# Kernel tuning notes

Hardware: AMD Instinct MI355X
Metric: run time of the kernel (lower is better)

Reference implementation:

```python
import jax, jax.numpy as jnp
import numpy as np

HEADS = 16
D_MODEL = 1024
HEAD_DIM = D_MODEL // HEADS


def setup_inputs() -> dict:
    key = jax.random.key(0)
    ks = jax.random.split(key, 11)
    B, S = 4, 2048
    scale_in = 1.0 / np.sqrt(HEAD_DIM)
    scale_out = 1.0 / np.sqrt(D_MODEL)
    return {
        "values": jax.random.normal(ks[0], (B, S, D_MODEL), dtype=jnp.float32),
        "keys": jax.random.normal(ks[1], (B, S, D_MODEL), dtype=jnp.float32),
        "query": jax.random.normal(ks[2], (B, S, D_MODEL), dtype=jnp.float32),
        "wq": jax.random.normal(ks[3], (HEAD_DIM, HEAD_DIM), dtype=jnp.float32) * scale_in,
        "bq": jax.random.normal(ks[4], (HEAD_DIM,), dtype=jnp.float32) * 0.01,
        "wk": jax.random.normal(ks[5], (HEAD_DIM, HEAD_DIM), dtype=jnp.float32) * scale_in,
        "bk": jax.random.normal(ks[6], (HEAD_DIM,), dtype=jnp.float32) * 0.01,
        "wv": jax.random.normal(ks[7], (HEAD_DIM, HEAD_DIM), dtype=jnp.float32) * scale_in,
        "bv": jax.random.normal(ks[8], (HEAD_DIM,), dtype=jnp.float32) * 0.01,
        "wo": jax.random.normal(ks[9], (D_MODEL, D_MODEL), dtype=jnp.float32) * scale_out,
        "bo": jax.random.normal(ks[10], (D_MODEL,), dtype=jnp.float32) * 0.01,
    }


def reference(values, keys, query, wq, bq, wk, bk, wv, bv, wo, bo):
    B, Sq = query.shape[0], query.shape[1]
    Sk, Sv = keys.shape[1], values.shape[1]
    # reshape to (n, s, h, d); per-head linear shares one [d,d] weight across heads
    v = values.reshape(B, Sv, HEADS, HEAD_DIM) @ wv.T + bv
    k = keys.reshape(B, Sk, HEADS, HEAD_DIM) @ wk.T + bk
    q = query.reshape(B, Sq, HEADS, HEAD_DIM) @ wq.T + bq
    # scores scaled by sqrt(d_model) (as in original, NOT sqrt(head_dim))
    energy = jnp.einsum("nqhd,nkhd->nhqk", q, k)
    attn = jax.nn.softmax(energy / jnp.sqrt(jnp.float32(D_MODEL)), axis=-1)
    out = jnp.einsum("nhqk,nkhd->nqhd", attn, v).reshape(B, Sq, D_MODEL)
    return out @ wo.T + bo
```

## Files before the change

### kernel.cpp

```cpp
#include <hip/hip_runtime.h>

typedef unsigned short u16;
typedef short  bfrag  __attribute__((ext_vector_type(8), may_alias));
typedef unsigned long long ull_a __attribute__((may_alias));
typedef int    int_a  __attribute__((may_alias));
typedef int    i4_a   __attribute__((ext_vector_type(4), may_alias));
typedef float  f4_a   __attribute__((ext_vector_type(4), may_alias));
typedef __attribute__((ext_vector_type(4)))  float facc4;
typedef __attribute__((ext_vector_type(16))) float facc16;

#define SEQ   2048
#define NHEAD 16
#define HD    64
#define DM    1024
#define BH    64
#define NTOK  8192
#define QSC   0.04508422f

#if defined(__has_builtin)
#if __has_builtin(__builtin_amdgcn_cvt_pk_bf16_f32)
#define HAS_CVT_PK 1
#endif
#endif
#ifndef HAS_CVT_PK
#define HAS_CVT_PK 0
#endif

__device__ __forceinline__ u16 f2bf(float f){
  union { float f; unsigned u; } x; x.f = f;
  unsigned r = x.u + 0x7FFFu + ((x.u >> 16) & 1u);
  return (u16)(r >> 16);
}
__device__ __forceinline__ unsigned pk2(float a, float b){
#if HAS_CVT_PK
  auto r = __builtin_amdgcn_cvt_pk_bf16_f32(a, b);
  union { decltype(r) v; unsigned u; } x; x.v = r; return x.u;
#else
  return (unsigned)f2bf(a) | ((unsigned)f2bf(b) << 16);
#endif
}
__device__ __forceinline__ unsigned long long pk4(float a, float b, float c, float d){
  return (unsigned long long)pk2(a,b) | ((unsigned long long)pk2(c,d) << 32);
}
__device__ __forceinline__ bfrag ld8f(const float* p){
  f4_a a = *(const f4_a*)p;
  f4_a b = *(const f4_a*)(p + 4);
  union { bfrag v; unsigned u[4]; } r;
  r.u[0] = pk2(a[0],a[1]); r.u[1] = pk2(a[2],a[3]);
  r.u[2] = pk2(b[0],b[1]); r.u[3] = pk2(b[2],b[3]);
  return r.v;
}
__device__ __forceinline__ void stage16(const u16* g, u16* l){
  __builtin_amdgcn_global_load_lds((const __attribute__((address_space(1))) void*)g,
                                   (__attribute__((address_space(3))) void*)l, 16, 0, 0);
}

__global__ __launch_bounds__(256) void k_wconv(
  const float* __restrict__ wo, const float* __restrict__ wq,
  const float* __restrict__ wk, const float* __restrict__ wv,
  u16* __restrict__ dst)
{
  long i = ((long)blockIdx.x * 256 + threadIdx.x) * 8;
  const float* src; long off;
  if      (i < 1048576)        { src = wo; off = i; }
  else if (i < 1048576+4096)   { src = wq; off = i - 1048576; }
  else if (i < 1048576+8192)   { src = wk; off = i - (1048576+4096); }
  else                         { src = wv; off = i - (1048576+8192); }
  f4_a a = *(const f4_a*)(src + off);
  f4_a b = *(const f4_a*)(src + off + 4);
  ull_a* p = (ull_a*)(dst + i);
  p[0] = pk4(a[0],a[1],a[2],a[3]);
  p[1] = pk4(b[0],b[1],b[2],b[3]);
}

__global__ __launch_bounds__(256) void k_proj(
  const float* __restrict__ vin, const float* __restrict__ kin, const float* __restrict__ qin,
  const u16* __restrict__ wqb, const u16* __restrict__ wkb, const u16* __restrict__ wvb,
  const float* __restrict__ bq, const float* __restrict__ bk, const float* __restrict__ bv,
  u16* __restrict__ qo, u16* __restrict__ ko, u16* __restrict__ vo)
{
  __shared__ __align__(16) u16 Lq[16*264], Lk[16*264], Lv[16*264];
  int tid  = threadIdx.x;
  int wid  = tid >> 6, lane = tid & 63;
  int quad = lane >> 4, col = lane & 15;
  int token = blockIdx.x * 4 + wid;
  int b  = (blockIdx.x * 4) >> 11;
  int s0 = (blockIdx.x * 4) & 2047;
  long xbase = (long)token * DM;

  bfrag aq[2], ak[2], av[2];
  #pragma unroll
  for (int ks = 0; ks < 2; ks++){
    long off = xbase + (long)col * HD + ks*32 + quad*8;
    aq[ks] = ld8f(qin + off);
    ak[ks] = ld8f(kin + off);
    av[ks] = ld8f(vin + off);
  }
  #pragma unroll
  for (int ns = 0; ns < 4; ns++){
    facc4 accq = {0.f,0.f,0.f,0.f}, acck = {0.f,0.f,0.f,0.f}, accv = {0.f,0.f,0.f,0.f};
    #pragma unroll
    for (int ks = 0; ks < 2; ks++){
      int woff = (ns*16 + col) * HD + ks*32 + quad*8;
      bfrag bwq = *(const bfrag*)(wqb + woff);
      bfrag bwk = *(const bfrag*)(wkb + woff);
      bfrag bwv = *(const bfrag*)(wvb + woff);
      accq = __builtin_amdgcn_mfma_f32_16x16x32_bf16(aq[ks], bwq, accq, 0,0,0);
      acck = __builtin_amdgcn_mfma_f32_16x16x32_bf16(ak[ks], bwk, acck, 0,0,0);
      accv = __builtin_amdgcn_mfma_f32_16x16x32_bf16(av[ks], bwv, accv, 0,0,0);
    }
    int d = ns*16 + col;
    float fbq = bq[d], fbk = bk[d], fbv = bv[d];
    #pragma unroll
    for (int r = 0; r < 4; r++){
      int h = quad*4 + r;
      int li = h*264 + wid*64 + d;
      Lq[li] = f2bf((accq[r] + fbq) * QSC);
      Lk[li] = f2bf(acck[r] + fbk);
      Lv[li] = f2bf(accv[r] + fbv);
    }
  }
  __syncthreads();
  int h = tid >> 4, c = tid & 15;
  int src = h*264 + c*16;
  long gb = ((long)(b*NHEAD + h) * SEQ + s0) * HD + c*16;
  *(i4_a*)(qo + gb)     = *(const i4_a*)&Lq[src];
  *(i4_a*)(qo + gb + 8) = *(const i4_a*)&Lq[src + 8];
  *(i4_a*)(ko + gb)     = *(const i4_a*)&Lk[src];
  *(i4_a*)(ko + gb + 8) = *(const i4_a*)&Lk[src + 8];
  *(i4_a*)(vo + gb)     = *(const i4_a*)&Lv[src];
  *(i4_a*)(vo + gb + 8) = *(const i4_a*)&Lv[src + 8];
}

__global__ __launch_bounds__(256) void k_vtrans(
  const u16* __restrict__ vin, u16* __restrict__ vt)
{
  __shared__ __align__(16) u16 T[64*264];
  int tid = threadIdx.x;
  int wid = tid >> 6, lane = tid & 63;
  int s0  = blockIdx.x * 256;
  int bh  = blockIdx.y;
  const u16* ip = vin + ((long)bh * SEQ + s0 + tid) * HD;
  #pragma unroll
  for (int j = 0; j < 8; j++){
    bfrag v8 = *(const bfrag*)(ip + j*8);
    #pragma unroll
    for (int i = 0; i < 8; i++)
      T[(j*8 + i)*264 + tid] = (u16)((short*)&v8)[i];
  }
  __syncthreads();
  long obase = (long)bh * HD * SEQ + s0;
  #pragma unroll
  for (int it = 0; it < 16; it++){
    int d = it*4 + wid;
    ull_a v = *(const ull_a*)&T[d*264 + lane*4];
    *(ull_a*)(vt + obase + (long)d * SEQ + lane*4) = v;
  }
}

__global__ __launch_bounds__(256, 3) void k_attn(
  const u16* __restrict__ qws, const u16* __restrict__ kws, const u16* __restrict__ vt,
  u16* __restrict__ aout)
{
  __shared__ __align__(16) u16 KV[2][2][64*64];
  __shared__ __align__(16) u16 Pt[4][32*72];
  int tid = threadIdx.x;
  int wid = tid >> 6, lane = tid & 63;
  int ln = lane & 31, hh = lane >> 5;
  int bh = blockIdx.y;
  int q0 = blockIdx.x * 128 + wid * 32;
  long base = (long)bh * SEQ * HD;

  int srow   = lane >> 3;
  int schunk = (lane & 7) ^ srow;

  bfrag qf[4];
  #pragma unroll
  for (int ks = 0; ks < 4; ks++)
    qf[ks] = *(const bfrag*)(qws + base + (long)(q0 + ln)*HD + ks*16 + hh*8);

  facc16 OO0, OO1;
  #pragma unroll
  for (int r = 0; r < 16; r++){ OO0[r] = 0.f; OO1[r] = 0.f; }
  float l_ = 0.f;

  #pragma unroll
  for (int g2 = 0; g2 < 2; g2++){
    int g = wid + g2*4;
    stage16(kws + base + (long)(g*8 + srow)*HD + schunk*8,       &KV[0][0][g*512]);
    stage16(vt  + base + (long)(g*8 + srow)*SEQ + schunk*8,      &KV[0][1][g*512]);
  }

  for (int kt = 0; kt < 32; kt++){
    int buf = kt & 1;
    __syncthreads();
    if (kt + 1 < 32){
      int k0n = (kt + 1) * 64;
      #pragma unroll
      for (int g2 = 0; g2 < 2; g2++){
        int g = wid + g2*4;
        stage16(kws + base + (long)(k0n + g*8 + srow)*HD + schunk*8, &KV[buf^1][0][g*512]);
        stage16(vt  + base + (long)(g*8 + srow)*SEQ + k0n + schunk*8, &KV[buf^1][1][g*512]);
      }
    }

    facc16 E0, E1;
    #pragma unroll
    for (int r = 0; r < 16; r++){ E0[r] = 0.f; E1[r] = 0.f; }
    #pragma unroll
    for (int ks = 0; ks < 4; ks++){
      int sw = ((2*ks + hh) ^ (ln & 7)) * 8;
      bfrag kf0 = *(const bfrag*)&KV[buf][0][ ln      *64 + sw];
      bfrag kf1 = *(const bfrag*)&KV[buf][0][(32 + ln)*64 + sw];
      E0 = __builtin_amdgcn_mfma_f32_32x32x16_bf16(kf0, qf[ks], E0, 0,0,0);
      E1 = __builtin_amdgcn_mfma_f32_32x32x16_bf16(kf1, qf[ks], E1, 0,0,0);
    }

    float rs = 0.f;
    #pragma unroll
    for (int r = 0; r < 16; r++){
      float p0 = __builtin_amdgcn_exp2f(E0[r]);
      float p1 = __builtin_amdgcn_exp2f(E1[r]);
      E0[r] = p0; E1[r] = p1; rs += p0 + p1;
    }
    rs += __shfl_xor(rs, 32, 64);
    l_ += rs;

    u16* pw = &Pt[wid][ln*72];
    #pragma unroll
    for (int g = 0; g < 4; g++){
      *(ull_a*)(pw +      8*g + 4*hh) = pk4(E0[4*g], E0[4*g+1], E0[4*g+2], E0[4*g+3]);
      *(ull_a*)(pw + 32 + 8*g + 4*hh) = pk4(E1[4*g], E1[4*g+1], E1[4*g+2], E1[4*g+3]);
    }

    bfrag pf[4];
    #pragma unroll
    for (int ks = 0; ks < 4; ks++)
      pf[ks] = *(const bfrag*)&Pt[wid][ln*72 + ks*16 + hh*8];
    #pragma unroll
    for (int ks = 0; ks < 4; ks++){
      int sw = ((2*ks + hh) ^ (ln & 7)) * 8;
      bfrag vf0 = *(const bfrag*)&KV[buf][1][ ln      *64 + sw];
      bfrag vf1 = *(const bfrag*)&KV[buf][1][(32 + ln)*64 + sw];
      OO0 = __builtin_amdgcn_mfma_f32_32x32x16_bf16(vf0, pf[ks], OO0, 0,0,0);
      OO1 = __builtin_amdgcn_mfma_f32_32x32x16_bf16(vf1, pf[ks], OO1, 0,0,0);
    }
  }

  float inv = 1.0f / l_;
  int b_ = bh >> 4, h_ = bh & 15;
  long orow = ((long)(b_ * SEQ + q0 + ln) * NHEAD + h_) * HD;
  #pragma unroll
  for (int g = 0; g < 4; g++){
    *(ull_a*)(aout + orow +      8*g + 4*hh) =
      pk4(OO0[4*g]*inv, OO0[4*g+1]*inv, OO0[4*g+2]*inv, OO0[4*g+3]*inv);
    *(ull_a*)(aout + orow + 32 + 8*g + 4*hh) =
      pk4(OO1[4*g]*inv, OO1[4*g+1]*inv, OO1[4*g+2]*inv, OO1[4*g+3]*inv);
  }
}

__global__ __launch_bounds__(256) void k_oproj(
  const u16* __restrict__ A, const u16* __restrict__ Bw,
  const float* __restrict__ bo, float* __restrict__ out)
{
  __shared__ __align__(16) u16 As[128*64];
  __shared__ __align__(16) u16 Bs[128*64];
  int tid  = threadIdx.x;
  int wid  = tid >> 6, lane = tid & 63;
  int quad = lane >> 4, col = lane & 15;
  int m0 = blockIdx.x * 128;
  int n0 = blockIdx.y * 128;
  int wm = (wid & 1) * 64, wn = (wid >> 1) * 64;

  facc4 acc[4][4];
  #pragma unroll
  for (int i = 0; i < 4; i++)
    #pragma unroll
    for (int j = 0; j < 4; j++) acc[i][j] = {0.f,0.f,0.f,0.f};

  int srow = wid*8 + (lane >> 3);
  int scol = (lane & 7) * 8;
  const u16* Ag = A  + (long)(m0 + srow) * DM + scol;
  const u16* Bg = Bw + (long)(n0 + srow) * DM + scol;

  for (int k0 = 0; k0 < DM; k0 += 64){
    __syncthreads();
    #pragma unroll
    for (int j = 0; j < 4; j++){
      stage16(Ag + (long)j*32*DM + k0, &As[(j*32 + wid*8)*64]);
      stage16(Bg + (long)j*32*DM + k0, &Bs[(j*32 + wid*8)*64]);
    }
    __syncthreads();

    #pragma unroll
    for (int ks = 0; ks < 2; ks++){
      bfrag af[4], bf[4];
      #pragma unroll
      for (int i = 0; i < 4; i++)
        af[i] = *(const bfrag*)&As[(wm + i*16 + col)*64 + ks*32 + quad*8];
      #pragma unroll
      for (int i = 0; i < 4; i++)
        bf[i] = *(const bfrag*)&Bs[(wn + i*16 + col)*64 + ks*32 + quad*8];
      #pragma unroll
      for (int i = 0; i < 4; i++)
        #pragma unroll
        for (int j = 0; j < 4; j++)
          acc[i][j] = __builtin_amdgcn_mfma_f32_16x16x32_bf16(af[i], bf[j], acc[i][j], 0,0,0);
    }
  }

  #pragma unroll
  for (int j = 0; j < 4; j++){
    int n = n0 + wn + j*16 + col;
    float bias = bo[n];
    #pragma unroll
    for (int i = 0; i < 4; i++){
      long mrow = m0 + wm + i*16 + quad*4;
      #pragma unroll
      for (int r = 0; r < 4; r++)
        out[(mrow + r) * DM + n] = acc[i][j][r] + bias;
    }
  }
}

extern "C" void kernel_launch(void* const* d_in, const int* in_sizes, int n_in,
                              void* d_out, int out_size, void* d_ws, size_t ws_size,
                              hipStream_t stream)
{
  const float* values = (const float*)d_in[0];
  const float* keys   = (const float*)d_in[1];
  const float* query  = (const float*)d_in[2];
  const float* wq = (const float*)d_in[3];
  const float* bq = (const float*)d_in[4];
  const float* wk = (const float*)d_in[5];
  const float* bk = (const float*)d_in[6];
  const float* wv = (const float*)d_in[7];
  const float* bv = (const float*)d_in[8];
  const float* wo = (const float*)d_in[9];
  const float* bo = (const float*)d_in[10];

  const long N = 8388608;
  u16* qws  = (u16*)d_ws;
  u16* kws  = qws  + N;
  u16* vws  = kws  + N;
  u16* vtws = vws  + N;
  u16* wob  = vtws + N;
  u16* wqb  = wob + 1048576;
  u16* wkb  = wqb + 4096;
  u16* wvb  = wkb + 4096;
  u16* aws  = vws;

  k_wconv <<<518,           256, 0, stream>>>(wo, wq, wk, wv, wob);
  k_proj  <<<2048,          256, 0, stream>>>(values, keys, query, wqb, wkb, wvb,
                                              bq, bk, bv, qws, kws, vws);
  k_vtrans<<<dim3(8, 64),   256, 0, stream>>>(vws, vtws);
  k_attn  <<<dim3(16, 64),  256, 0, stream>>>(qws, kws, vtws, aws);
  k_oproj <<<dim3(64, 8),   256, 0, stream>>>(aws, wob, bo, (float*)d_out);
}
```

Baseline: 324.1 us.

## Build P operand in registers via permlane32 swap instead of LDS round-trip

The softmax probabilities are now repacked into the bf16 MFMA B-operand layout entirely in registers, using permlane32_swap (or a shuffle fallback) in place of writing to and reading back from a per-wave LDS tile. This removes the Pt shared buffer, its LDS traffic and its LDS footprint. The per-tile row-sum shuffle is deferred to a single reduction after the loop. Occupancy is raised to 4 blocks per CU and s_setprio brackets the MFMA sections; the higher occupancy target may increase register pressure or cause spills.

New measurement: 308.5 us. -4.8%, faster.

```diff
diff --git a/kernel.cpp b/kernel.cpp
--- a/kernel.cpp
+++ b/kernel.cpp
@@ -6,6 +6,7 @@
 typedef int    int_a  __attribute__((may_alias));
 typedef int    i4_a   __attribute__((ext_vector_type(4), may_alias));
 typedef float  f4_a   __attribute__((ext_vector_type(4), may_alias));
+typedef unsigned u32x2 __attribute__((ext_vector_type(2)));
 typedef __attribute__((ext_vector_type(4)))  float facc4;
 typedef __attribute__((ext_vector_type(16))) float facc16;
 
@@ -21,9 +22,15 @@
 #if __has_builtin(__builtin_amdgcn_cvt_pk_bf16_f32)
 #define HAS_CVT_PK 1
 #endif
+#if __has_builtin(__builtin_amdgcn_permlane32_swap)
+#define HAS_PLSWAP 1
+#endif
 #endif
 #ifndef HAS_CVT_PK
 #define HAS_CVT_PK 0
+#endif
+#ifndef HAS_PLSWAP
+#define HAS_PLSWAP 0
 #endif
 
 __device__ __forceinline__ u16 f2bf(float f){
@@ -41,6 +48,19 @@
 }
 __device__ __forceinline__ unsigned long long pk4(float a, float b, float c, float d){
   return (unsigned long long)pk2(a,b) | ((unsigned long long)pk2(c,d) << 32);
+}
+__device__ __forceinline__ void swap32(unsigned &a, unsigned &b){
+#if HAS_PLSWAP
+  u32x2 r = __builtin_amdgcn_permlane32_swap(a, b, false, false);
+  a = r[0]; b = r[1];
+#else
+  int lane = threadIdx.x & 63; int hh = lane >> 5;
+  unsigned pa = (unsigned)__shfl_xor((int)a, 32, 64);
+  unsigned pb = (unsigned)__shfl_xor((int)b, 32, 64);
+  unsigned na = hh ? pb : a;
+  unsigned nb = hh ? b  : pa;
+  a = na; b = nb;
+#endif
 }
 __device__ __forceinline__ bfrag ld8f(const float* p){
   f4_a a = *(const f4_a*)p;
@@ -158,12 +178,11 @@
   }
 }
 
-__global__ __launch_bounds__(256, 3) void k_attn(
+__global__ __launch_bounds__(256, 4) void k_attn(
   const u16* __restrict__ qws, const u16* __restrict__ kws, const u16* __restrict__ vt,
   u16* __restrict__ aout)
 {
   __shared__ __align__(16) u16 KV[2][2][64*64];
-  __shared__ __align__(16) u16 Pt[4][32*72];
   int tid = threadIdx.x;
   int wid = tid >> 6, lane = tid & 63;
   int ln = lane & 31, hh = lane >> 5;
@@ -207,6 +226,7 @@
     facc16 E0, E1;
     #pragma unroll
     for (int r = 0; r < 16; r++){ E0[r] = 0.f; E1[r] = 0.f; }
+    __builtin_amdgcn_s_setprio(1);
     #pragma unroll
     for (int ks = 0; ks < 4; ks++){
       int sw = ((2*ks + hh) ^ (ln & 7)) * 8;
@@ -215,6 +235,7 @@
       E0 = __builtin_amdgcn_mfma_f32_32x32x16_bf16(kf0, qf[ks], E0, 0,0,0);
       E1 = __builtin_amdgcn_mfma_f32_32x32x16_bf16(kf1, qf[ks], E1, 0,0,0);
     }
+    __builtin_amdgcn_s_setprio(0);
 
     float rs = 0.f;
     #pragma unroll
@@ -223,20 +244,28 @@
       float p1 = __builtin_amdgcn_exp2f(E1[r]);
       E0[r] = p0; E1[r] = p1; rs += p0 + p1;
     }
-    rs += __shfl_xor(rs, 32, 64);
     l_ += rs;
 
-    u16* pw = &Pt[wid][ln*72];
-    #pragma unroll
-    for (int g = 0; g < 4; g++){
-      *(ull_a*)(pw +      8*g + 4*hh) = pk4(E0[4*g], E0[4*g+1], E0[4*g+2], E0[4*g+3]);
-      *(ull_a*)(pw + 32 + 8*g + 4*hh) = pk4(E1[4*g], E1[4*g+1], E1[4*g+2], E1[4*g+3]);
-    }
-
     bfrag pf[4];
     #pragma unroll
-    for (int ks = 0; ks < 4; ks++)
-      pf[ks] = *(const bfrag*)&Pt[wid][ln*72 + ks*16 + hh*8];
+    for (int half = 0; half < 2; half++){
+      const facc16& P = half ? E1 : E0;
+      #pragma unroll
+      for (int k2 = 0; k2 < 2; k2++){
+        int rb = k2 * 8;
+        unsigned A0 = pk2(P[rb+0], P[rb+1]);
+        unsigned A1 = pk2(P[rb+2], P[rb+3]);
+        unsigned B0 = pk2(P[rb+4], P[rb+5]);
+        unsigned B1 = pk2(P[rb+6], P[rb+7]);
+        swap32(A0, B0);
+        swap32(A1, B1);
+        union { bfrag v; unsigned u[4]; } t;
+        t.u[0] = A0; t.u[1] = A1; t.u[2] = B0; t.u[3] = B1;
+        pf[half*2 + k2] = t.v;
+      }
+    }
+
+    __builtin_amdgcn_s_setprio(1);
     #pragma unroll
     for (int ks = 0; ks < 4; ks++){
       int sw = ((2*ks + hh) ^ (ln & 7)) * 8;
@@ -245,8 +274,10 @@
       OO0 = __builtin_amdgcn_mfma_f32_32x32x16_bf16(vf0, pf[ks], OO0, 0,0,0);
       OO1 = __builtin_amdgcn_mfma_f32_32x32x16_bf16(vf1, pf[ks], OO1, 0,0,0);
     }
-  }
-
+    __builtin_amdgcn_s_setprio(0);
+  }
+
+  l_ += __shfl_xor(l_, 32, 64);
   float inv = 1.0f / l_;
   int b_ = bh >> 4, h_ = bh & 15;
   long orow = ((long)(b_ * SEQ + q0 + ln) * NHEAD + h_) * HD;
```
